# Kernel optimization log

Measured on AMD Instinct MI355X. Metric: run time of the kernel, lower is better.

Reference implementation:

```python
import jax, jax.numpy as jnp
import numpy as np

NHEAD = 8
TOPKS = (8, 8)  # topk per level, coarse -> fine


def _to_bshd(x):
    # [B, C, H, W] -> [B, H*W, nhead, d]  (matches rearrange 'b c h w -> b (h w) c' + view)
    b, c, h, w = x.shape
    return jnp.transpose(x.reshape(b, c, h * w), (0, 2, 1)).reshape(b, h * w, NHEAD, c // NHEAD)


def _coarse_level(q, k, v, topk):
    b, c, h, w = k.shape
    d = c // NHEAD
    q_, k_, v_ = _to_bshd(q), _to_bshd(k), _to_bshd(v)
    temp = 1.0 / (d ** 0.5)
    A = jax.nn.softmax(jnp.einsum('nlhd,nshd->nlsh', q_, k_) * temp, axis=2)  # [b,L,S,h]
    _, idx = jax.lax.top_k(jnp.swapaxes(A, 2, 3), topk)  # [b,L,h,k]
    idx = jnp.swapaxes(idx, 2, 3)                        # [b,L,k,h]
    msg = jnp.einsum('nlsh,nshd->nlhd', A, v_)           # [b,L,h,d]
    topk_pos = jnp.stack([idx // w, idx % w])            # [2,b,L,k,h]
    return msg, topk_pos


def _fine_level(q, k, v, topk_pos, topk_prev, topk):
    b, c, h0, w0 = q.shape
    w1 = k.shape[3]
    d = c // NHEAD
    k_, v_ = _to_bshd(k), _to_bshd(v)
    H2, W2 = h0 // 2, w0 // 2
    L0 = H2 * W2
    # query grouped into 2x2 quads: [b, L0, 4, h, d]
    q_ = q.reshape(b, c, H2, 2, W2, 2).transpose(0, 2, 4, 3, 5, 1).reshape(b, L0, 4, NHEAD, d)
    tp = topk_pos * 2  # coarse positions -> fine grid
    cand = [(tp[0] + x) * w1 + tp[1] + y for x in (0, 1) for y in (0, 1)]
    t2 = topk_prev * 4
    idx = jnp.stack(cand, axis=3).reshape(b, L0, t2, NHEAD)  # [b,L,t2,h]
    idx_bh = idx.transpose(0, 3, 1, 2).reshape(b, NHEAD, L0 * t2)

    def gather(p):  # p: [b,S,h,d] -> gathered [b,L,t2,h,d]
        g = jnp.take_along_axis(jnp.swapaxes(p, 1, 2), idx_bh[..., None], axis=2)
        return g.reshape(b, NHEAD, L0, t2, d).transpose(0, 2, 3, 1, 4)

    tk, tv = gather(k_), gather(v_)
    temp = 1.0 / (d ** 0.5)
    A = jax.nn.softmax(jnp.einsum('blqhd,blthd->blqth', q_, tk) * temp, axis=3)  # [b,L,4,t2,h]
    _, ti = jax.lax.top_k(jnp.moveaxis(A, 3, 4), topk)  # [b,L,4,h,k]
    ti = jnp.moveaxis(ti, 4, 3)                         # [b,L,4,k,h]
    msg = jnp.einsum('blqth,blthd->blqhd', A, tv)       # [b,L,4,h,d]
    idx_b = jnp.broadcast_to(idx[:, :, None], (b, L0, 4, t2, NHEAD))
    gidx = jnp.take_along_axis(idx_b, ti, axis=3)       # [b,L,4,k,h] flat fine-grid indices
    gidx = gidx.reshape(b, H2, W2, 2, 2, topk, NHEAD).transpose(0, 1, 3, 2, 4, 5, 6)
    gidx = gidx.reshape(b, h0 * w0, topk, NHEAD)
    return msg, gidx


def _forward(q_fine, q_coarse, k_fine, k_coarse, v_fine, v_coarse, weight):
    msg0, topk_pos = _coarse_level(q_coarse, k_coarse, v_coarse, TOPKS[0])
    msg1, _ = _fine_level(q_fine, k_fine, v_fine, topk_pos, TOPKS[0], TOPKS[1])
    w = jax.nn.softmax(weight, axis=0)
    fm = msg0 * w[0]                  # [b,Lc,h,d]
    fm = fm[:, :, None] + msg1 * w[1]  # [b,Lc,4,h,d]
    b, Hc, Wc = q_coarse.shape[0], q_coarse.shape[2], q_coarse.shape[3]
    d = fm.shape[-1]
    # rearrange 'b (H W) (t1 t2) h d -> b (H t1 W t2) h d'
    fm = fm.reshape(b, Hc, Wc, 2, 2, NHEAD, d).transpose(0, 1, 3, 2, 4, 5, 6)
    return fm.reshape(b, Hc * Wc * 4, NHEAD, d)


def setup_inputs() -> dict:
    key = jax.random.key(0)
    ks = jax.random.split(key, 7)
    B, C = 4, 128
    return {
        'q_fine': jax.random.normal(ks[0], (B, C, 64, 64), jnp.float32),
        'q_coarse': jax.random.normal(ks[1], (B, C, 32, 32), jnp.float32),
        'k_fine': jax.random.normal(ks[2], (B, C, 64, 64), jnp.float32),
        'k_coarse': jax.random.normal(ks[3], (B, C, 32, 32), jnp.float32),
        'v_fine': jax.random.normal(ks[4], (B, C, 64, 64), jnp.float32),
        'v_coarse': jax.random.normal(ks[5], (B, C, 32, 32), jnp.float32),
        'weight': jax.random.normal(ks[6], (2,), jnp.float32),
    }


def reference(q_fine, q_coarse, k_fine, k_coarse, v_fine, v_coarse, weight):
    return _forward(q_fine, q_coarse, k_fine, k_coarse, v_fine, v_coarse, weight)
```

## Files before the change

### kernel.cpp

```cpp
#include <hip/hip_runtime.h>
#include <stdint.h>

#define TEMP 0.25f

__global__ __launch_bounds__(512, 2)
void coarse_kernel(const float* __restrict__ qc, const float* __restrict__ kc,
                   const float* __restrict__ vc, float* __restrict__ msg0,
                   int* __restrict__ topk_out)
{
    const int ltile = blockIdx.x;
    const int h     = blockIdx.y;
    const int b     = blockIdx.z;
    const int tid   = threadIdx.x;
    const int lane  = tid & 63;
    const int wv    = tid >> 6;
    const int lbase = ltile * 32;

    __shared__ float sKV[16 * 1024];

    const size_t base = (size_t)(b * 128 + h * 16) * 1024;

    {
        const float4* gK = (const float4*)(kc + base);
        float4* lK = (float4*)sKV;
        #pragma unroll
        for (int i = 0; i < 8; ++i) lK[tid + 512 * i] = gK[tid + 512 * i];
    }

    float qreg[4];
    {
        int dq = lane & 15;
        #pragma unroll
        for (int li = 0; li < 4; ++li){
            int l = lbase + wv * 4 + li;
            qreg[li] = qc[base + (size_t)dq * 1024 + l] * TEMP;
        }
    }
    __syncthreads();

    float p[4][16];
    #pragma unroll
    for (int li = 0; li < 4; ++li)
        #pragma unroll
        for (int j = 0; j < 16; ++j) p[li][j] = 0.f;

    #pragma unroll
    for (int dch = 0; dch < 16; ++dch){
        float kf[16];
        #pragma unroll
        for (int ch = 0; ch < 4; ++ch){
            float4 kv = *(const float4*)&sKV[dch * 1024 + ch * 256 + (lane << 2)];
            kf[ch*4+0] = kv.x; kf[ch*4+1] = kv.y;
            kf[ch*4+2] = kv.z; kf[ch*4+3] = kv.w;
        }
        float qs[4];
        #pragma unroll
        for (int li = 0; li < 4; ++li) qs[li] = __shfl(qreg[li], dch);
        #pragma unroll
        for (int li = 0; li < 4; ++li)
            #pragma unroll
            for (int j = 0; j < 16; ++j)
                p[li][j] = fmaf(qs[li], kf[j], p[li][j]);
    }

    float invs[4];
    #pragma unroll
    for (int li = 0; li < 4; ++li){
        float m = p[li][0];
        #pragma unroll
        for (int j = 1; j < 16; ++j) m = fmaxf(m, p[li][j]);
        #pragma unroll
        for (int off = 32; off > 0; off >>= 1) m = fmaxf(m, __shfl_xor(m, off));
        float s = 0.f;
        #pragma unroll
        for (int j = 0; j < 16; ++j){ p[li][j] = __expf(p[li][j] - m); s += p[li][j]; }
        #pragma unroll
        for (int off = 32; off > 0; off >>= 1) s += __shfl_xor(s, off);
        invs[li] = 1.0f / s;
    }

    __syncthreads();
    {
        const float4* gV = (const float4*)(vc + base);
        float4* lV = (float4*)sKV;
        #pragma unroll
        for (int i = 0; i < 8; ++i) lV[tid + 512 * i] = gV[tid + 512 * i];
    }
    __syncthreads();

    float outv = 0.f;
    #pragma unroll
    for (int dd = 0; dd < 16; ++dd){
        float vf[16];
        #pragma unroll
        for (int ch = 0; ch < 4; ++ch){
            float4 vv = *(const float4*)&sKV[dd * 1024 + ch * 256 + (lane << 2)];
            vf[ch*4+0] = vv.x; vf[ch*4+1] = vv.y;
            vf[ch*4+2] = vv.z; vf[ch*4+3] = vv.w;
        }
        float a[4];
        #pragma unroll
        for (int li = 0; li < 4; ++li){
            float s = 0.f;
            #pragma unroll
            for (int j = 0; j < 16; ++j) s = fmaf(p[li][j], vf[j], s);
            a[li] = s;
        }
        #pragma unroll
        for (int off = 32; off > 0; off >>= 1)
            #pragma unroll
            for (int li = 0; li < 4; ++li) a[li] += __shfl_xor(a[li], off);
        #pragma unroll
        for (int li = 0; li < 4; ++li)
            outv = (lane == li * 16 + dd) ? a[li] * invs[li] : outv;
    }
    {
        int li = lane >> 4, dd = lane & 15;
        int l = lbase + wv * 4 + li;
        msg0[(size_t)((b * 1024 + l) * 8 + h) * 16 + dd] = outv;
    }

    const int lanebase = lane << 4;
    int mytk = 0;
    for (int r = 0; r < 8; ++r){
        float bv[4]; int bi[4];
        #pragma unroll
        for (int li = 0; li < 4; ++li){
            float v0[8]; int j0[8];
            #pragma unroll
            for (int k = 0; k < 8; ++k){
                bool g = p[li][2*k+1] > p[li][2*k];
                v0[k] = g ? p[li][2*k+1] : p[li][2*k];
                j0[k] = g ? 2*k+1 : 2*k;
            }
            float v1[4]; int j1[4];
            #pragma unroll
            for (int k = 0; k < 4; ++k){
                bool g = v0[2*k+1] > v0[2*k];
                v1[k] = g ? v0[2*k+1] : v0[2*k];
                j1[k] = g ? j0[2*k+1] : j0[2*k];
            }
            float v2[2]; int j2[2];
            #pragma unroll
            for (int k = 0; k < 2; ++k){
                bool g = v1[2*k+1] > v1[2*k];
                v2[k] = g ? v1[2*k+1] : v1[2*k];
                j2[k] = g ? j1[2*k+1] : j1[2*k];
            }
            bool g3 = v2[1] > v2[0];
            bv[li] = g3 ? v2[1] : v2[0];
            bi[li] = lanebase | (g3 ? j2[1] : j2[0]);
        }
        #pragma unroll
        for (int off = 32; off > 0; off >>= 1){
            #pragma unroll
            for (int li = 0; li < 4; ++li){
                float ov = __shfl_xor(bv[li], off);
                int   oi = __shfl_xor(bi[li], off);
                bool g = (ov > bv[li]) || (ov == bv[li] && oi < bi[li]);
                bv[li] = g ? ov : bv[li];
                bi[li] = g ? oi : bi[li];
            }
        }
        #pragma unroll
        for (int li = 0; li < 4; ++li){
            #pragma unroll
            for (int j = 0; j < 16; ++j)
                p[li][j] = (bi[li] == (lanebase | j)) ? -1.0f : p[li][j];
            mytk = (lane == li * 8 + r) ? bi[li] : mytk;
        }
    }
    if (lane < 32){
        int li = lane >> 3, r = lane & 7;
        int jw = mytk & 15, lw = mytk >> 4;
        int s = ((jw >> 2) << 8) | (lw << 2) | (jw & 3);
        int l = lbase + wv * 4 + li;
        topk_out[((b * 1024 + l) * 8 + h) * 8 + r] = s;
    }
}

__global__ __launch_bounds__(256)
void transpose_kernel(const float* __restrict__ kf, const float* __restrict__ vf,
                      const float* __restrict__ qf,
                      float* __restrict__ kT, float* __restrict__ vT,
                      float* __restrict__ qT)
{
    const int pt = blockIdx.x;
    const int b  = blockIdx.y;
    const int z  = blockIdx.z;
    const float* src = (z == 0) ? kf : (z == 1) ? vf : qf;
    float*       dst = (z == 0) ? kT : (z == 1) ? vT : qT;
    const int tid = threadIdx.x;
    __shared__ float tile[64][129];
    const int pos0 = pt * 64;

    #pragma unroll
    for (int it = 0; it < 8; ++it){
        int task = it * 256 + tid;
        int ch = task >> 4, p4 = task & 15;
        float4 v = *(const float4*)(src + (size_t)(b * 128 + ch) * 4096 + pos0 + p4 * 4);
        tile[p4*4+0][ch] = v.x; tile[p4*4+1][ch] = v.y;
        tile[p4*4+2][ch] = v.z; tile[p4*4+3][ch] = v.w;
    }
    __syncthreads();
    #pragma unroll
    for (int it = 0; it < 8; ++it){
        int task = it * 256 + tid;
        int p = task >> 5, c4 = task & 31;
        float4 v = make_float4(tile[p][c4*4+0], tile[p][c4*4+1],
                               tile[p][c4*4+2], tile[p][c4*4+3]);
        *(float4*)(dst + ((size_t)(b * 4096) + pos0 + p) * 128 + c4 * 4) = v;
    }
}

__global__ __launch_bounds__(256)
void fine_kernel(const float* __restrict__ qf, const float* __restrict__ kf,
                 const float* __restrict__ vf,
                 const float* __restrict__ qTg, const float* __restrict__ kTg,
                 const float* __restrict__ vTg, int transposed,
                 const float* __restrict__ wt,
                 const int* __restrict__ topk_in, const float* __restrict__ msg0,
                 float* __restrict__ out)
{
    const int l0 = blockIdx.x;
    const int b  = blockIdx.y;
    const int tid = threadIdx.x;

    __shared__ float vT[8][16][34];
    __shared__ float qT[8][4][16];
    __shared__ float pT[8][4][32];
    __shared__ int tkS[8][8];

    if (tid < 64) tkS[tid >> 3][tid & 7] =
        topk_in[((b * 1024 + l0) * 8 + (tid >> 3)) * 8 + (tid & 7)];
    __syncthreads();

    const int i = l0 >> 5, j = l0 & 31;
    const int hh = tid >> 5;
    const int t  = tid & 31;
    const int kk = t >> 2, cp = t & 3;

    float k[16];
    {
        int s   = tkS[hh][kk];
        int pos = (2 * (s >> 5) + (cp >> 1)) * 64 + 2 * (s & 31) + (cp & 1);
        if (transposed){
            size_t gb = ((size_t)(b * 4096) + pos) * 128 + hh * 16;
            const float4* kp = (const float4*)(kTg + gb);
            float4 k0 = kp[0], k1 = kp[1], k2 = kp[2], k3 = kp[3];
            k[0]=k0.x; k[1]=k0.y; k[2]=k0.z; k[3]=k0.w;
            k[4]=k1.x; k[5]=k1.y; k[6]=k1.z; k[7]=k1.w;
            k[8]=k2.x; k[9]=k2.y; k[10]=k2.z; k[11]=k2.w;
            k[12]=k3.x; k[13]=k3.y; k[14]=k3.z; k[15]=k3.w;
            const float4* vp = (const float4*)(vTg + gb);
            float4 v0 = vp[0], v1 = vp[1], v2 = vp[2], v3 = vp[3];
            vT[hh][0][t]=v0.x;  vT[hh][1][t]=v0.y;  vT[hh][2][t]=v0.z;  vT[hh][3][t]=v0.w;
            vT[hh][4][t]=v1.x;  vT[hh][5][t]=v1.y;  vT[hh][6][t]=v1.z;  vT[hh][7][t]=v1.w;
            vT[hh][8][t]=v2.x;  vT[hh][9][t]=v2.y;  vT[hh][10][t]=v2.z; vT[hh][11][t]=v2.w;
            vT[hh][12][t]=v3.x; vT[hh][13][t]=v3.y; vT[hh][14][t]=v3.z; vT[hh][15][t]=v3.w;
        } else {
            size_t gb = (size_t)(b * 128 + hh * 16) * 4096 + pos;
            #pragma unroll
            for (int ch = 0; ch < 16; ++ch){
                k[ch] = kf[gb + (size_t)ch * 4096];
                vT[hh][ch][t] = vf[gb + (size_t)ch * 4096];
            }
        }
    }
    if (tid < 128){
        int qh = tid >> 4, aq = (tid >> 2) & 3, c4 = tid & 3;
        int qpos = (2 * i + (aq >> 1)) * 64 + 2 * j + (aq & 1);
        if (transposed){
            float4 u = *(const float4*)(qTg + ((size_t)(b * 4096) + qpos) * 128 + qh * 16 + c4 * 4);
            qT[qh][aq][c4*4+0] = u.x * TEMP;
            qT[qh][aq][c4*4+1] = u.y * TEMP;
            qT[qh][aq][c4*4+2] = u.z * TEMP;
            qT[qh][aq][c4*4+3] = u.w * TEMP;
        } else {
            #pragma unroll
            for (int c = 0; c < 4; ++c)
                qT[qh][aq][c4*4+c] =
                    qf[(size_t)(b * 128 + qh * 16 + c4 * 4 + c) * 4096 + qpos] * TEMP;
        }
    }
    __syncthreads();

    {
        float sc[4] = {0.f, 0.f, 0.f, 0.f};
        #pragma unroll
        for (int dch = 0; dch < 16; ++dch){
            float kv = k[dch];
            #pragma unroll
            for (int q = 0; q < 4; ++q) sc[q] = fmaf(qT[hh][q][dch], kv, sc[q]);
        }
        #pragma unroll
        for (int q = 0; q < 4; ++q){
            float m = sc[q];
            #pragma unroll
            for (int off = 16; off > 0; off >>= 1) m = fmaxf(m, __shfl_xor(m, off, 32));
            float e = __expf(sc[q] - m);
            float s = e;
            #pragma unroll
            for (int off = 16; off > 0; off >>= 1) s += __shfl_xor(s, off, 32);
            pT[hh][q][t] = e / s;
        }
    }
    __syncthreads();

    {
        float w0 = wt[0], w1 = wt[1];
        float mx = fmaxf(w0, w1);
        float e0 = __expf(w0 - mx), e1 = __expf(w1 - mx);
        float w0f = e0 / (e0 + e1), w1f = e1 / (e0 + e1);

        int q0 = (tid >> 4) & 1;
        int dd = tid & 15;
        float a0 = 0.f, a1 = 0.f;
        #pragma unroll
        for (int tt = 0; tt < 16; ++tt){
            float v0 = vT[hh][dd][tt * 2], v1 = vT[hh][dd][tt * 2 + 1];
            float2 pA = *(const float2*)&pT[hh][q0][tt * 2];
            float2 pB = *(const float2*)&pT[hh][q0 + 2][tt * 2];
            a0 = fmaf(pA.x, v0, a0); a0 = fmaf(pA.y, v1, a0);
            a1 = fmaf(pB.x, v0, a1); a1 = fmaf(pB.y, v1, a1);
        }
        float m0 = msg0[(size_t)((b * 1024 + l0) * 8 + hh) * 16 + dd];
        float o0 = w0f * m0 + w1f * a0;
        float o1 = w0f * m0 + w1f * a1;
        int posA = (2 * i) * 64 + 2 * j + q0;
        int posB = (2 * i + 1) * 64 + 2 * j + q0;
        out[(size_t)((b * 4096 + posA) * 8 + hh) * 16 + dd] = o0;
        out[(size_t)((b * 4096 + posB) * 8 + hh) * 16 + dd] = o1;
    }
}

extern "C" void kernel_launch(void* const* d_in, const int* in_sizes, int n_in,
                              void* d_out, int out_size, void* d_ws, size_t ws_size,
                              hipStream_t stream)
{
    (void)in_sizes; (void)n_in; (void)out_size;

    const float* q_fine   = (const float*)d_in[0];
    const float* q_coarse = (const float*)d_in[1];
    const float* k_fine   = (const float*)d_in[2];
    const float* k_coarse = (const float*)d_in[3];
    const float* v_fine   = (const float*)d_in[4];
    const float* v_coarse = (const float*)d_in[5];
    const float* weight   = (const float*)d_in[6];

    const size_t MB = 1024 * 1024;
    float* msg0 = (float*)d_ws;
    int*   topk = (int*)((char*)d_ws + 2 * MB);
    float* kT   = (float*)((char*)d_ws + 3 * MB);
    float* vT   = (float*)((char*)d_ws + 11 * MB);
    float* qT   = (float*)((char*)d_ws + 19 * MB);
    const int doT = (ws_size >= 27 * MB) ? 1 : 0;

    if (doT){
        dim3 gt(64, 4, 3);
        transpose_kernel<<<gt, dim3(256), 0, stream>>>(k_fine, v_fine, q_fine, kT, vT, qT);
    }

    dim3 g1(32, 8, 4);
    coarse_kernel<<<g1, dim3(512), 0, stream>>>(q_coarse, k_coarse, v_coarse, msg0, topk);

    dim3 g2(1024, 4);
    fine_kernel<<<g2, dim3(256), 0, stream>>>(q_fine, k_fine, v_fine,
                                              qT, kT, vT, doT,
                                              weight, topk, msg0, (float*)d_out);
}
```

Before: 227.2 us.

## Pack fine K/V as interleaved bf16 in quad-grouped layout for gather

The pre-pass kernel now converts fine K and V to bf16 and writes them interleaved per head, with the four pixels of each 2x2 quad stored contiguously. Each thread in the fine kernel then fetches its K and V slice with one contiguous 64-byte read instead of two separate 64-byte fp32 reads from different buffers. This halves gather traffic and workspace and improves locality. In exchange, K and V are rounded to bf16, which lowers attention precision and can change top-k selection.

```diff
diff --git a/kernel.cpp b/kernel.cpp
--- a/kernel.cpp
+++ b/kernel.cpp
@@ -2,6 +2,18 @@
 #include <stdint.h>
 
 #define TEMP 0.25f
+
+static __device__ __forceinline__ uint32_t f2b_bits(float f){
+    union { float f; uint32_t i; } x; x.f = f;
+    uint32_t u = x.i;
+    return (u + 0x7FFFu + ((u >> 16) & 1u)) >> 16;
+}
+static __device__ __forceinline__ float bl(uint32_t u){
+    union { uint32_t i; float f; } x; x.i = u << 16; return x.f;
+}
+static __device__ __forceinline__ float bh(uint32_t u){
+    union { uint32_t i; float f; } x; x.i = u & 0xffff0000u; return x.f;
+}
 
 __global__ __launch_bounds__(512, 2)
 void coarse_kernel(const float* __restrict__ qc, const float* __restrict__ kc,
@@ -180,16 +192,14 @@
 }
 
 __global__ __launch_bounds__(256)
-void transpose_kernel(const float* __restrict__ kf, const float* __restrict__ vf,
-                      const float* __restrict__ qf,
-                      float* __restrict__ kT, float* __restrict__ vT,
-                      float* __restrict__ qT)
+void pack_kernel(const float* __restrict__ kf, const float* __restrict__ vf,
+                 const float* __restrict__ qf,
+                 uint32_t* __restrict__ packed, float* __restrict__ qT)
 {
     const int pt = blockIdx.x;
     const int b  = blockIdx.y;
     const int z  = blockIdx.z;
     const float* src = (z == 0) ? kf : (z == 1) ? vf : qf;
-    float*       dst = (z == 0) ? kT : (z == 1) ? vT : qT;
     const int tid = threadIdx.x;
     __shared__ float tile[64][129];
     const int pos0 = pt * 64;
@@ -203,21 +213,43 @@
         tile[p4*4+2][ch] = v.z; tile[p4*4+3][ch] = v.w;
     }
     __syncthreads();
-    #pragma unroll
-    for (int it = 0; it < 8; ++it){
-        int task = it * 256 + tid;
-        int p = task >> 5, c4 = task & 31;
-        float4 v = make_float4(tile[p][c4*4+0], tile[p][c4*4+1],
-                               tile[p][c4*4+2], tile[p][c4*4+3]);
-        *(float4*)(dst + ((size_t)(b * 4096) + pos0 + p) * 128 + c4 * 4) = v;
+
+    if (z == 2){
+        #pragma unroll
+        for (int it = 0; it < 8; ++it){
+            int task = it * 256 + tid;
+            int p = task >> 5, c4 = task & 31;
+            float4 v = make_float4(tile[p][c4*4+0], tile[p][c4*4+1],
+                                   tile[p][c4*4+2], tile[p][c4*4+3]);
+            *(float4*)(qT + ((size_t)(b * 4096) + pos0 + p) * 128 + c4 * 4) = v;
+        }
+    } else {
+        const int x = pt;
+        #pragma unroll
+        for (int it = 0; it < 2; ++it){
+            int task = it * 256 + tid;
+            int h = task >> 6, y = task & 63;
+            int pprime = ((x >> 1) * 32 + (y >> 1)) * 4 + (x & 1) * 2 + (y & 1);
+            size_t line = (size_t)(b * 8 + h) * 4096 + pprime;
+            uint32_t dw[8];
+            #pragma unroll
+            for (int i = 0; i < 8; ++i){
+                uint32_t lo = f2b_bits(tile[y][h * 16 + 2 * i]);
+                uint32_t hi = f2b_bits(tile[y][h * 16 + 2 * i + 1]);
+                dw[i] = lo | (hi << 16);
+            }
+            uint4* dst4 = (uint4*)packed + line * 4 + z * 2;
+            dst4[0] = make_uint4(dw[0], dw[1], dw[2], dw[3]);
+            dst4[1] = make_uint4(dw[4], dw[5], dw[6], dw[7]);
+        }
     }
 }
 
 __global__ __launch_bounds__(256)
 void fine_kernel(const float* __restrict__ qf, const float* __restrict__ kf,
                  const float* __restrict__ vf,
-                 const float* __restrict__ qTg, const float* __restrict__ kTg,
-                 const float* __restrict__ vTg, int transposed,
+                 const float* __restrict__ qTg, const uint32_t* __restrict__ packed,
+                 int transposed,
                  const float* __restrict__ wt,
                  const int* __restrict__ topk_in, const float* __restrict__ msg0,
                  float* __restrict__ out)
@@ -242,23 +274,26 @@
 
     float k[16];
     {
-        int s   = tkS[hh][kk];
-        int pos = (2 * (s >> 5) + (cp >> 1)) * 64 + 2 * (s & 31) + (cp & 1);
+        int s = tkS[hh][kk];
         if (transposed){
-            size_t gb = ((size_t)(b * 4096) + pos) * 128 + hh * 16;
-            const float4* kp = (const float4*)(kTg + gb);
-            float4 k0 = kp[0], k1 = kp[1], k2 = kp[2], k3 = kp[3];
-            k[0]=k0.x; k[1]=k0.y; k[2]=k0.z; k[3]=k0.w;
-            k[4]=k1.x; k[5]=k1.y; k[6]=k1.z; k[7]=k1.w;
-            k[8]=k2.x; k[9]=k2.y; k[10]=k2.z; k[11]=k2.w;
-            k[12]=k3.x; k[13]=k3.y; k[14]=k3.z; k[15]=k3.w;
-            const float4* vp = (const float4*)(vTg + gb);
-            float4 v0 = vp[0], v1 = vp[1], v2 = vp[2], v3 = vp[3];
-            vT[hh][0][t]=v0.x;  vT[hh][1][t]=v0.y;  vT[hh][2][t]=v0.z;  vT[hh][3][t]=v0.w;
-            vT[hh][4][t]=v1.x;  vT[hh][5][t]=v1.y;  vT[hh][6][t]=v1.z;  vT[hh][7][t]=v1.w;
-            vT[hh][8][t]=v2.x;  vT[hh][9][t]=v2.y;  vT[hh][10][t]=v2.z; vT[hh][11][t]=v2.w;
-            vT[hh][12][t]=v3.x; vT[hh][13][t]=v3.y; vT[hh][14][t]=v3.z; vT[hh][15][t]=v3.w;
+            const uint4* pk = (const uint4*)packed;
+            size_t line = (size_t)(b * 8 + hh) * 4096 + s * 4 + cp;
+            uint4 a0 = pk[line*4+0], a1 = pk[line*4+1];
+            uint4 a2 = pk[line*4+2], a3 = pk[line*4+3];
+            k[0]=bl(a0.x);  k[1]=bh(a0.x);  k[2]=bl(a0.y);  k[3]=bh(a0.y);
+            k[4]=bl(a0.z);  k[5]=bh(a0.z);  k[6]=bl(a0.w);  k[7]=bh(a0.w);
+            k[8]=bl(a1.x);  k[9]=bh(a1.x);  k[10]=bl(a1.y); k[11]=bh(a1.y);
+            k[12]=bl(a1.z); k[13]=bh(a1.z); k[14]=bl(a1.w); k[15]=bh(a1.w);
+            vT[hh][0][t]=bl(a2.x);  vT[hh][1][t]=bh(a2.x);
+            vT[hh][2][t]=bl(a2.y);  vT[hh][3][t]=bh(a2.y);
+            vT[hh][4][t]=bl(a2.z);  vT[hh][5][t]=bh(a2.z);
+            vT[hh][6][t]=bl(a2.w);  vT[hh][7][t]=bh(a2.w);
+            vT[hh][8][t]=bl(a3.x);  vT[hh][9][t]=bh(a3.x);
+            vT[hh][10][t]=bl(a3.y); vT[hh][11][t]=bh(a3.y);
+            vT[hh][12][t]=bl(a3.z); vT[hh][13][t]=bh(a3.z);
+            vT[hh][14][t]=bl(a3.w); vT[hh][15][t]=bh(a3.w);
         } else {
+            int pos = (2 * (s >> 5) + (cp >> 1)) * 64 + 2 * (s & 31) + (cp & 1);
             size_t gb = (size_t)(b * 128 + hh * 16) * 4096 + pos;
             #pragma unroll
             for (int ch = 0; ch < 16; ++ch){
@@ -349,16 +384,15 @@
     const float* weight   = (const float*)d_in[6];
 
     const size_t MB = 1024 * 1024;
-    float* msg0 = (float*)d_ws;
-    int*   topk = (int*)((char*)d_ws + 2 * MB);
-    float* kT   = (float*)((char*)d_ws + 3 * MB);
-    float* vT   = (float*)((char*)d_ws + 11 * MB);
-    float* qT   = (float*)((char*)d_ws + 19 * MB);
-    const int doT = (ws_size >= 27 * MB) ? 1 : 0;
+    float*    msg0   = (float*)d_ws;
+    int*      topk   = (int*)((char*)d_ws + 2 * MB);
+    float*    qT     = (float*)((char*)d_ws + 3 * MB);
+    uint32_t* packed = (uint32_t*)((char*)d_ws + 11 * MB);
+    const int doT = (ws_size >= 19 * MB) ? 1 : 0;
 
     if (doT){
         dim3 gt(64, 4, 3);
-        transpose_kernel<<<gt, dim3(256), 0, stream>>>(k_fine, v_fine, q_fine, kT, vT, qT);
+        pack_kernel<<<gt, dim3(256), 0, stream>>>(k_fine, v_fine, q_fine, packed, qT);
     }
 
     dim3 g1(32, 8, 4);
@@ -366,6 +400,6 @@
 
     dim3 g2(1024, 4);
     fine_kernel<<<g2, dim3(256), 0, stream>>>(q_fine, k_fine, v_fine,
-                                              qT, kT, vT, doT,
+                                              qT, packed, doT,
                                               weight, topk, msg0, (float*)d_out);
 }
```

Measured after the change: 219.9 us. -3.2%, faster.
